# Optimization experiments

Hardware: AMD Instinct MI355X
Metric: run time of the kernel (lower is better)

## Reference

```python
import jax, jax.numpy as jnp
import numpy as np

MIN_FP16 = -65504.0  # torch.finfo(torch.float16).min
D_MODEL = 2048
NUM_HEAD = 16
HEAD_SIZE = D_MODEL // NUM_HEAD


def setup_inputs() -> dict:
    key = jax.random.key(0)
    k1, k2, k3, k4, k5 = jax.random.split(key, 5)
    B, S, D = 4, 2048, D_MODEL
    scale_in = 1.0 / np.sqrt(D)
    return {
        "x": jax.random.normal(k1, (B, S, D), dtype=jnp.float32),
        # nn.Linear(d_model, 3*d_model): weight [3D, D], bias [3D]
        "w_proj": jax.random.normal(k2, (3 * D, D), dtype=jnp.float32) * scale_in,
        "b_proj": jax.random.normal(k3, (3 * D,), dtype=jnp.float32) * 0.01,
        # nn.Linear(d_model, d_model)
        "w_ff": jax.random.normal(k4, (D, D), dtype=jnp.float32) * scale_in,
        "b_ff": jax.random.normal(k5, (D,), dtype=jnp.float32) * 0.01,
    }


def reference(x, w_proj, b_proj, w_ff, b_ff):
    B, S, D = x.shape
    H, hs = NUM_HEAD, HEAD_SIZE
    # fused QKV projection: [B,S,3D]
    x_proj = jnp.einsum("bsd,ed->bse", x, w_proj) + b_proj
    # view [B,S,H,3*hs] -> [B,H,S,3*hs], split into q,k,v [B,H,S,hs]
    x_proj = x_proj.reshape(B, S, H, 3 * hs).transpose(0, 2, 1, 3)
    q, k, v = jnp.split(x_proj, 3, axis=-1)
    next_prefix_kv = jnp.stack((k, v))  # [2,B,H,S,hs]
    # scaled scores [B,H,S,S]
    scores = jnp.einsum("bhqd,bhkd->bhqk", q, k) / np.sqrt(hs)
    # causal mask (prefix_kv=None => tmp_len == seq_len, offset 0)
    causal = jnp.tril(jnp.ones((S, S), dtype=bool))
    scores = jnp.where(causal, scores, MIN_FP16)
    probs = jax.nn.softmax(scores, axis=-1)  # dropout p=0 (eval)
    attn_o = jnp.einsum("bhqk,bhkd->bhqd", probs, v)
    attn_o = attn_o.transpose(0, 2, 1, 3).reshape(B, S, D)
    ff_o = jnp.einsum("bsd,ed->bse", attn_o, w_ff) + b_ff
    return ff_o, next_prefix_kv
```

## Files before the change

kernel.cpp:

```cpp
#include <hip/hip_runtime.h>


using floatx4 = __attribute__((ext_vector_type(4))) float;
using short8  = __attribute__((ext_vector_type(8))) short;

#define MFMA_BF16(a, b, c) __builtin_amdgcn_mfma_f32_16x16x32_bf16((a), (b), (c), 0, 0, 0)

static __device__ __forceinline__ unsigned short f2bf(float f) {
    unsigned u = __float_as_uint(f);
    u += 0x7FFF + ((u >> 16) & 1);
    return (unsigned short)(u >> 16);
}
static __device__ __forceinline__ short8 cvt8(const float* p) {
    float4 a = ((const float4*)p)[0];
    float4 b = ((const float4*)p)[1];
    short8 r;
    r[0] = (short)f2bf(a.x); r[1] = (short)f2bf(a.y);
    r[2] = (short)f2bf(a.z); r[3] = (short)f2bf(a.w);
    r[4] = (short)f2bf(b.x); r[5] = (short)f2bf(b.y);
    r[6] = (short)f2bf(b.z); r[7] = (short)f2bf(b.w);
    return r;
}

static __device__ __forceinline__ void gld16(const void* g, const void* l) {
    unsigned loff = (unsigned)__builtin_amdgcn_readfirstlane((int)(unsigned)(uintptr_t)l);
    __builtin_amdgcn_global_load_lds(
        (__attribute__((address_space(1))) unsigned*)(uintptr_t)g,
        (__attribute__((address_space(3))) unsigned*)loff,
        16, 0, 0);
}

__global__ __launch_bounds__(256) void cvt_kernel(
    const float* __restrict__ X, const float* __restrict__ Wp,
    unsigned short* __restrict__ Xb, unsigned short* __restrict__ Wpb)
{
    const int NX = 2097152;
    const int NP = 1572864;
    const int total = NX + NP;
    const int stride = gridDim.x * 256;
    for (int g = blockIdx.x * 256 + threadIdx.x; g < total; g += stride) {
        const float* src; unsigned short* dst; int off;
        if (g < NX) { src = X;  dst = Xb;  off = g; }
        else        { src = Wp; dst = Wpb; off = g - NX; }
        const int row = off >> 8;
        const int c   = off & 255;
        const int dof = (row << 8) | (c & ~7) | ((c ^ row) & 7);
        short8 v = cvt8(src + (size_t)off * 8);
        *(short8*)(dst + (size_t)dof * 8) = v;
    }
}

__global__ __launch_bounds__(256) void gemm_qkv_kernel(
    const unsigned short* __restrict__ Xb,
    const unsigned short* __restrict__ Wpb,
    const float* __restrict__ Bias,
    unsigned short* __restrict__ Qws,
    float* __restrict__ KV)
{
    const int K = 2048;
    __shared__ unsigned short As[128 * 64];
    __shared__ unsigned short Bs[128 * 64];
    const int n0 = blockIdx.x * 128;
    const int m0 = blockIdx.y * 128;
    const int t = threadIdx.x;
    const int w = t >> 6, l = t & 63;
    const int lr = l & 15, lq = l >> 4;
    const int lr7 = lr & 7;
    const int wr = w >> 1, wc = w & 1;
    const int srow = l >> 3;
    const int scol = (l & 7) * 8;

    floatx4 acc[4][4];
#pragma unroll
    for (int mi = 0; mi < 4; ++mi)
#pragma unroll
        for (int ni = 0; ni < 4; ++ni) acc[mi][ni] = (floatx4){0, 0, 0, 0};

    for (int k0 = 0; k0 < K; k0 += 64) {
        __syncthreads();
#pragma unroll
        for (int i = 0; i < 4; ++i) {
            const int rb = (i * 4 + w) * 8;
            gld16(Xb  + (size_t)(m0 + rb + srow) * K + k0 + scol, &As[(rb)*64]);
            gld16(Wpb + (size_t)(n0 + rb + srow) * K + k0 + scol, &Bs[(rb)*64]);
        }
        __syncthreads();
#pragma unroll
        for (int kc = 0; kc < 2; ++kc) {
            short8 af[4], bg[4];
#pragma unroll
            for (int mi = 0; mi < 4; ++mi)
                af[mi] = *(const short8*)
                    &As[(wr * 64 + mi * 16 + lr) * 64 + ((((kc << 2) | lq) ^ lr7) << 3)];
#pragma unroll
            for (int ni = 0; ni < 4; ++ni)
                bg[ni] = *(const short8*)
                    &Bs[(wc * 64 + ni * 16 + lr) * 64 + ((((kc << 2) | lq) ^ lr7) << 3)];
#pragma unroll
            for (int mi = 0; mi < 4; ++mi)
#pragma unroll
                for (int ni = 0; ni < 4; ++ni)
                    acc[mi][ni] = MFMA_BF16(af[mi], bg[ni], acc[mi][ni]);
        }
    }
#pragma unroll
    for (int ni = 0; ni < 4; ++ni) {
        int e = n0 + wc * 64 + ni * 16 + lr;
        int h = e / 384;
        int c = e - h * 384;
        float bias = Bias[e];
#pragma unroll
        for (int mi = 0; mi < 4; ++mi) {
#pragma unroll
            for (int r = 0; r < 4; ++r) {
                int m = m0 + wr * 64 + mi * 16 + lq * 4 + r;
                int b = m >> 11, s = m & 2047;
                float o = acc[mi][ni][r] + bias;
                size_t base = (((size_t)(b * 16 + h)) * 2048 + s) * 128;
                if (c < 128)
                    Qws[base + ((((c >> 3) ^ (s & 7)) << 3) | (c & 7))] = f2bf(o);
                else if (c < 256) KV[base + (c - 128)] = o;
                else              KV[(size_t)16777216 + base + (c - 256)] = o;
            }
        }
    }
}

__global__ __launch_bounds__(256) void repack_kv_kernel(
    const float* __restrict__ KV,
    unsigned short* __restrict__ Kb,
    unsigned short* __restrict__ Vtb)
{
    __shared__ short Vt[128][72];
    const int bh = blockIdx.x >> 5;
    const int w  = blockIdx.x & 31;
    const int t  = threadIdx.x;

    {
        const int kr = t >> 2;
        const int c4 = (t & 3) * 4;
        const int s  = w * 64 + kr;
        const float* kp = KV + ((size_t)bh * 2048 + s) * 128 + c4 * 8;
        unsigned short* ko = Kb + ((size_t)bh * 2048 + s) * 128;
        const int sw = s & 7;
#pragma unroll
        for (int j = 0; j < 4; ++j) {
            short8 v = cvt8(kp + j * 8);
            *(short8*)(ko + ((c4 + j) ^ sw) * 8) = v;
        }
    }

    {
        const int vkp = t & 31;
        const int vd0 = (t >> 5) * 16;
        const float* vap = KV + (((size_t)64 + bh) * 2048 + w * 64 + 2 * vkp) * 128 + vd0;
        short8 va0 = cvt8(vap),       va1 = cvt8(vap + 8);
        short8 vb0 = cvt8(vap + 128), vb1 = cvt8(vap + 136);
#pragma unroll
        for (int dd = 0; dd < 8; ++dd) {
            unsigned w0 = (unsigned)(unsigned short)va0[dd] |
                          ((unsigned)(unsigned short)vb0[dd] << 16);
            unsigned w1 = (unsigned)(unsigned short)va1[dd] |
                          ((unsigned)(unsigned short)vb1[dd] << 16);
            *(unsigned*)&Vt[vd0 + dd][2 * vkp]     = w0;
            *(unsigned*)&Vt[vd0 + 8 + dd][2 * vkp] = w1;
        }
    }
    __syncthreads();
    {
        const int d = t >> 1, hf = t & 1;
        unsigned short* vo = Vtb + ((size_t)bh * 128 + d) * 2048 + w * 64;
        const int dw = d & 7;
#pragma unroll
        for (int j = 0; j < 4; ++j) {
            int c = hf * 4 + j;
            uint4 v = *(const uint4*)&Vt[d][c * 8];
            *(uint4*)(vo + (c ^ dw) * 8) = v;
        }
    }
}

__global__ __launch_bounds__(256) void attn_kernel(
    unsigned short* __restrict__ QA,
    const unsigned short* __restrict__ Kb,
    const unsigned short* __restrict__ Vtb)
{
    const int S = 2048;
    __shared__ unsigned short Ks[2][64 * 128];
    __shared__ unsigned short Vt[2][128 * 64];
    __shared__ short Pb[4][16][72];

    const int bh = blockIdx.y;
    const int qt = gridDim.x - 1 - blockIdx.x;
    const int q0 = qt * 64;
    const int t = threadIdx.x;
    const int wv = t >> 6;
    const int l = t & 63;
    const int lr = l & 15;
    const int lq = l >> 4;
    const int lr7 = lr & 7;

    unsigned short* Qp = QA + ((size_t)bh * S + q0) * 128;
    const unsigned short* gK = Kb + (size_t)bh * S * 128;
    const unsigned short* gV = Vtb + (size_t)bh * 128 * S;

    short8 qf[4];
#pragma unroll
    for (int kc = 0; kc < 4; ++kc)
        qf[kc] = *(const short8*)(Qp + (size_t)(wv * 16 + lr) * 128 +
                                  ((((kc << 2) | lq) ^ lr7) << 3));

    float m_i = -1e30f, l_i = 0.0f;
    floatx4 oacc[8];
#pragma unroll
    for (int nt = 0; nt < 8; ++nt) oacc[nt] = (floatx4){0, 0, 0, 0};

    const int ntiles = qt + 1;

#define STAGE(BUF, KV0)                                                        \
    {                                                                          \
        const int kv0_ = (KV0);                                                \
        _Pragma("unroll")                                                      \
        for (int i = 0; i < 4; ++i) {                                          \
            const int off = (i * 16 + wv * 4) * 128;                           \
            gld16(gK + (size_t)kv0_ * 128 + off + l * 8, &Ks[BUF][off]);       \
        }                                                                      \
        _Pragma("unroll")                                                      \
        for (int i = 0; i < 4; ++i) {                                          \
            const int ob = (i * 16 + wv * 4) * 256 + l * 16;                   \
            const int d = ob >> 7, rem = ob & 127;                             \
            gld16((const char*)gV + (size_t)d * (S * 2) + kv0_ * 2 + rem,      \
                  (const char*)&Vt[BUF][0] + (i * 16 + wv * 4) * 256);         \
        }                                                                      \
    }

    STAGE(0, 0);

    for (int it = 0; it < ntiles; ++it) {
        const int cur = it & 1;
        __syncthreads();
        if (it + 1 < ntiles) STAGE(cur ^ 1, (it + 1) * 64);

        const unsigned short* Kc = &Ks[cur][0];
        const unsigned short* Vc = &Vt[cur][0];

        floatx4 sacc[4];
#pragma unroll
        for (int mt = 0; mt < 4; ++mt) sacc[mt] = (floatx4){0, 0, 0, 0};
#pragma unroll
        for (int kc = 0; kc < 4; ++kc) {
#pragma unroll
            for (int mt = 0; mt < 4; ++mt) {
                short8 a = *(const short8*)
                    &Kc[(mt * 16 + lr) * 128 + ((((kc << 2) | lq) ^ lr7) << 3)];
                sacc[mt] = MFMA_BF16(a, qf[kc], sacc[mt]);
            }
        }

        float sv[16];
        const bool diag = (it == qt);
#pragma unroll
        for (int mt = 0; mt < 4; ++mt)
#pragma unroll
            for (int r = 0; r < 4; ++r) {
                float x = sacc[mt][r] * 0.08838834764831845f;
                if (diag && (mt * 16 + lq * 4 + r > wv * 16 + lr)) x = -1e30f;
                sv[mt * 4 + r] = x;
            }
        float mx = sv[0];
#pragma unroll
        for (int j = 1; j < 16; ++j) mx = fmaxf(mx, sv[j]);
        mx = fmaxf(mx, __shfl_xor(mx, 16));
        mx = fmaxf(mx, __shfl_xor(mx, 32));
        float m_new = fmaxf(m_i, mx);
        float alpha = __expf(m_i - m_new);
        m_i = m_new;
        float sum = 0.0f;
        unsigned pw[8];
#pragma unroll
        for (int j = 0; j < 8; ++j) {
            float p0 = __expf(sv[2 * j]     - m_new);
            float p1 = __expf(sv[2 * j + 1] - m_new);
            sum += p0 + p1;
            pw[j] = (unsigned)f2bf(p0) | ((unsigned)f2bf(p1) << 16);
        }
        sum += __shfl_xor(sum, 16);
        sum += __shfl_xor(sum, 32);
        l_i = l_i * alpha + sum;

#pragma unroll
        for (int mt = 0; mt < 4; ++mt)
            *(uint2*)&Pb[wv][lr][mt * 16 + lq * 4] =
                make_uint2(pw[2 * mt], pw[2 * mt + 1]);

        float am[4];
#pragma unroll
        for (int r = 0; r < 4; ++r) am[r] = __shfl(alpha, lq * 4 + r);
#pragma unroll
        for (int nt = 0; nt < 8; ++nt)
#pragma unroll
            for (int r = 0; r < 4; ++r) oacc[nt][r] *= am[r];

        short8 pa0 = *(const short8*)&Pb[wv][lr][lq * 8];
        short8 pa1 = *(const short8*)&Pb[wv][lr][32 + lq * 8];
#pragma unroll
        for (int nt = 0; nt < 8; ++nt) {
            const int row = nt * 16 + lr;
            short8 v0 = *(const short8*)&Vc[row * 64 + ((lq ^ lr7) << 3)];
            short8 v1 = *(const short8*)&Vc[row * 64 + (((4 + lq) ^ lr7) << 3)];
            oacc[nt] = MFMA_BF16(pa0, v0, oacc[nt]);
            oacc[nt] = MFMA_BF16(pa1, v1, oacc[nt]);
        }
    }
#undef STAGE

    float lm[4];
#pragma unroll
    for (int r = 0; r < 4; ++r) lm[r] = 1.0f / __shfl(l_i, lq * 4 + r);
#pragma unroll
    for (int nt = 0; nt < 8; ++nt) {
#pragma unroll
        for (int r = 0; r < 4; ++r) {
            int q = wv * 16 + lq * 4 + r;
            int ch = (nt * 2 + (lr >> 3)) ^ (q & 7);
            Qp[(size_t)q * 128 + (ch << 3) + (lr & 7)] = f2bf(oacc[nt][r] * lm[r]);
        }
    }
}

__global__ __launch_bounds__(256) void gemm_ff_kernel(
    const unsigned short* __restrict__ AOhm,
    const float* __restrict__ W,
    const float* __restrict__ Bias,
    float* __restrict__ Out)
{
    const int K = 2048;
    __shared__ unsigned short As[128 * 64];
    __shared__ unsigned short Bs[128 * 64];
    const int n0 = blockIdx.x * 128;
    const int m0 = blockIdx.y * 128;
    const int t = threadIdx.x;
    const int w = t >> 6, l = t & 63;
    const int lr = l & 15, lq = l >> 4;
    const int lr7 = lr & 7;
    const int wr = w >> 1, wc = w & 1;
    const int srow = l >> 3;
    const int scol = (l & 7) * 8;

    const int brow = t >> 1;
    const int bch0 = (t & 1) * 4;
    const int bsw  = brow & 7;
    const float* gB = W + (size_t)(n0 + brow) * K + bch0 * 8;

    floatx4 acc[4][4];
#pragma unroll
    for (int mi = 0; mi < 4; ++mi)
#pragma unroll
        for (int ni = 0; ni < 4; ++ni) acc[mi][ni] = (floatx4){0, 0, 0, 0};

    for (int k0 = 0; k0 < K; k0 += 64) {
        short8 bc[4];
#pragma unroll
        for (int j = 0; j < 4; ++j) bc[j] = cvt8(gB + k0 + j * 8);

        const int h = k0 >> 7, d0 = (k0 & 127) + scol;
        __syncthreads();
#pragma unroll
        for (int i = 0; i < 4; ++i) {
            const int rb = (i * 4 + w) * 8;
            const int m = m0 + rb + srow;
            const int b = m >> 11, s = m & 2047;
            gld16(AOhm + ((size_t)(b * 16 + h) * 2048 + s) * 128 + d0, &As[(rb)*64]);
        }
#pragma unroll
        for (int j = 0; j < 4; ++j)
            *(short8*)&Bs[brow * 64 + (((bch0 + j) ^ bsw) << 3)] = bc[j];
        __syncthreads();
#pragma unroll
        for (int kc = 0; kc < 2; ++kc) {
            short8 af[4], bg[4];
#pragma unroll
            for (int mi = 0; mi < 4; ++mi)
                af[mi] = *(const short8*)
                    &As[(wr * 64 + mi * 16 + lr) * 64 + ((((kc << 2) | lq) ^ lr7) << 3)];
#pragma unroll
            for (int ni = 0; ni < 4; ++ni)
                bg[ni] = *(const short8*)
                    &Bs[(wc * 64 + ni * 16 + lr) * 64 + ((((kc << 2) | lq) ^ lr7) << 3)];
#pragma unroll
            for (int mi = 0; mi < 4; ++mi)
#pragma unroll
                for (int ni = 0; ni < 4; ++ni)
                    acc[mi][ni] = MFMA_BF16(af[mi], bg[ni], acc[mi][ni]);
        }
    }
#pragma unroll
    for (int ni = 0; ni < 4; ++ni) {
        int e = n0 + wc * 64 + ni * 16 + lr;
        float bias = Bias[e];
#pragma unroll
        for (int mi = 0; mi < 4; ++mi) {
#pragma unroll
            for (int r = 0; r < 4; ++r) {
                int m = m0 + wr * 64 + mi * 16 + lq * 4 + r;
                Out[(size_t)m * 2048 + e] = acc[mi][ni][r] + bias;
            }
        }
    }
}

extern "C" void kernel_launch(void* const* d_in, const int* in_sizes, int n_in,
                              void* d_out, int out_size, void* d_ws, size_t ws_size,
                              hipStream_t stream) {
    const float* X  = (const float*)d_in[0];
    const float* Wp = (const float*)d_in[1];
    const float* bp = (const float*)d_in[2];
    const float* Wf = (const float*)d_in[3];
    const float* bf = (const float*)d_in[4];

    float* out = (float*)d_out;
    float* kv  = out + 16777216;
    unsigned short* Qws = (unsigned short*)d_ws;

    unsigned short* Xb  = (unsigned short*)out;
    unsigned short* Wpb = Xb + 16777216;
    unsigned short* Kbs = (unsigned short*)out;
    unsigned short* Vtb = Kbs + 16777216;

    cvt_kernel<<<dim3(2048), 256, 0, stream>>>(X, Wp, Xb, Wpb);
    gemm_qkv_kernel<<<dim3(48, 64), 256, 0, stream>>>(Xb, Wpb, bp, Qws, kv);
    repack_kv_kernel<<<dim3(2048), 256, 0, stream>>>(kv, Kbs, Vtb);
    attn_kernel<<<dim3(32, 64), 256, 0, stream>>>(Qws, Kbs, Vtb);
    gemm_ff_kernel<<<dim3(16, 64), 256, 0, stream>>>(Qws, Wf, bf, out);
}
```

Baseline: 962.4 us.

## Pre-convert FF weights to bf16, add lazy softmax rescale, packed bf16 conversion

Several changes land together. The cvt kernel now also converts w_ff to swizzled bf16 in workspace when there is room, so the FF GEMM can load both operands with global-to-LDS copies instead of converting fp32 on the fly; the old kernel is kept as a fallback. Attention skips the output rescale when the wave's new row max is within 8 of the running max (lazy rescaling) and uses hardware packed bf16 conversion. K/V staging addresses are precomputed as incrementing offsets. The lazy rescale allows unnormalised exponentials up to e^8, which slightly changes numerics but should stay within bf16 range.

Result: faster. 887.8 us (-7.8%).

```diff
diff --git a/kernel.cpp b/kernel.cpp
--- a/kernel.cpp
+++ b/kernel.cpp
@@ -1,4 +1,5 @@
 #include <hip/hip_runtime.h>
+#include <hip/hip_bf16.h>
 
 
 using floatx4 = __attribute__((ext_vector_type(4))) float;
@@ -11,15 +12,18 @@
     u += 0x7FFF + ((u >> 16) & 1);
     return (unsigned short)(u >> 16);
 }
+static __device__ __forceinline__ unsigned cvtpk(float lo, float hi) {
+    union { __hip_bfloat162 h; unsigned u; } r;
+    r.h = __float22bfloat162_rn(make_float2(lo, hi));
+    return r.u;
+}
 static __device__ __forceinline__ short8 cvt8(const float* p) {
     float4 a = ((const float4*)p)[0];
     float4 b = ((const float4*)p)[1];
-    short8 r;
-    r[0] = (short)f2bf(a.x); r[1] = (short)f2bf(a.y);
-    r[2] = (short)f2bf(a.z); r[3] = (short)f2bf(a.w);
-    r[4] = (short)f2bf(b.x); r[5] = (short)f2bf(b.y);
-    r[6] = (short)f2bf(b.z); r[7] = (short)f2bf(b.w);
-    return r;
+    union { unsigned u[4]; short8 s; } r;
+    r.u[0] = cvtpk(a.x, a.y); r.u[1] = cvtpk(a.z, a.w);
+    r.u[2] = cvtpk(b.x, b.y); r.u[3] = cvtpk(b.z, b.w);
+    return r.s;
 }
 
 static __device__ __forceinline__ void gld16(const void* g, const void* l) {
@@ -32,16 +36,20 @@
 
 __global__ __launch_bounds__(256) void cvt_kernel(
     const float* __restrict__ X, const float* __restrict__ Wp,
-    unsigned short* __restrict__ Xb, unsigned short* __restrict__ Wpb)
+    const float* __restrict__ Wf,
+    unsigned short* __restrict__ Xb, unsigned short* __restrict__ Wpb,
+    unsigned short* __restrict__ Wfb, int doWf)
 {
     const int NX = 2097152;
     const int NP = 1572864;
-    const int total = NX + NP;
+    const int NF = 524288;
+    const int total = NX + NP + (doWf ? NF : 0);
     const int stride = gridDim.x * 256;
     for (int g = blockIdx.x * 256 + threadIdx.x; g < total; g += stride) {
         const float* src; unsigned short* dst; int off;
-        if (g < NX) { src = X;  dst = Xb;  off = g; }
-        else        { src = Wp; dst = Wpb; off = g - NX; }
+        if (g < NX)           { src = X;  dst = Xb;  off = g; }
+        else if (g < NX + NP) { src = Wp; dst = Wpb; off = g - NX; }
+        else                  { src = Wf; dst = Wfb; off = g - NX - NP; }
         const int row = off >> 8;
         const int c   = off & 255;
         const int dof = (row << 8) | (c & ~7) | ((c ^ row) & 7);
@@ -215,31 +223,33 @@
 #pragma unroll
     for (int nt = 0; nt < 8; ++nt) oacc[nt] = (floatx4){0, 0, 0, 0};
 
-    const int ntiles = qt + 1;
-
-#define STAGE(BUF, KV0)                                                        \
+    const unsigned short* gKl = gK + l * 8;
+    const char* gVl = (const char*)gV + (size_t)((l >> 3) * 4096 + (l & 7) * 16);
+    size_t tK = 0, tV = 0;
+
+#define STAGE(BUF)                                                             \
     {                                                                          \
-        const int kv0_ = (KV0);                                                \
         _Pragma("unroll")                                                      \
         for (int i = 0; i < 4; ++i) {                                          \
             const int off = (i * 16 + wv * 4) * 128;                           \
-            gld16(gK + (size_t)kv0_ * 128 + off + l * 8, &Ks[BUF][off]);       \
+            gld16(gKl + tK + off, &Ks[BUF][off]);                              \
         }                                                                      \
         _Pragma("unroll")                                                      \
         for (int i = 0; i < 4; ++i) {                                          \
-            const int ob = (i * 16 + wv * 4) * 256 + l * 16;                   \
-            const int d = ob >> 7, rem = ob & 127;                             \
-            gld16((const char*)gV + (size_t)d * (S * 2) + kv0_ * 2 + rem,      \
+            const int vb = (i * 32 + wv * 8) * 4096;                           \
+            gld16(gVl + tV + vb,                                               \
                   (const char*)&Vt[BUF][0] + (i * 16 + wv * 4) * 256);         \
         }                                                                      \
     }
 
-    STAGE(0, 0);
+    const int ntiles = qt + 1;
+    STAGE(0);
+    tK += 8192; tV += 128;
 
     for (int it = 0; it < ntiles; ++it) {
         const int cur = it & 1;
         __syncthreads();
-        if (it + 1 < ntiles) STAGE(cur ^ 1, (it + 1) * 64);
+        if (it + 1 < ntiles) { STAGE(cur ^ 1); tK += 8192; tV += 128; }
 
         const unsigned short* Kc = &Ks[cur][0];
         const unsigned short* Vc = &Vt[cur][0];
@@ -272,17 +282,28 @@
         for (int j = 1; j < 16; ++j) mx = fmaxf(mx, sv[j]);
         mx = fmaxf(mx, __shfl_xor(mx, 16));
         mx = fmaxf(mx, __shfl_xor(mx, 32));
-        float m_new = fmaxf(m_i, mx);
-        float alpha = __expf(m_i - m_new);
-        m_i = m_new;
+        const bool nores = __all(mx <= m_i + 8.0f) != 0;
+        float alpha = 1.0f;
+        if (!nores) {
+            float m_new = fmaxf(m_i, mx);
+            alpha = __expf(m_i - m_new);
+            m_i = m_new;
+            float am[4];
+#pragma unroll
+            for (int r = 0; r < 4; ++r) am[r] = __shfl(alpha, lq * 4 + r);
+#pragma unroll
+            for (int nt = 0; nt < 8; ++nt)
+#pragma unroll
+                for (int r = 0; r < 4; ++r) oacc[nt][r] *= am[r];
+        }
         float sum = 0.0f;
         unsigned pw[8];
 #pragma unroll
         for (int j = 0; j < 8; ++j) {
-            float p0 = __expf(sv[2 * j]     - m_new);
-            float p1 = __expf(sv[2 * j + 1] - m_new);
+            float p0 = __expf(sv[2 * j]     - m_i);
+            float p1 = __expf(sv[2 * j + 1] - m_i);
             sum += p0 + p1;
-            pw[j] = (unsigned)f2bf(p0) | ((unsigned)f2bf(p1) << 16);
+            pw[j] = cvtpk(p0, p1);
         }
         sum += __shfl_xor(sum, 16);
         sum += __shfl_xor(sum, 32);
@@ -292,14 +313,6 @@
         for (int mt = 0; mt < 4; ++mt)
             *(uint2*)&Pb[wv][lr][mt * 16 + lq * 4] =
                 make_uint2(pw[2 * mt], pw[2 * mt + 1]);
-
-        float am[4];
-#pragma unroll
-        for (int r = 0; r < 4; ++r) am[r] = __shfl(alpha, lq * 4 + r);
-#pragma unroll
-        for (int nt = 0; nt < 8; ++nt)
-#pragma unroll
-            for (int r = 0; r < 4; ++r) oacc[nt][r] *= am[r];
 
         short8 pa0 = *(const short8*)&Pb[wv][lr][lq * 8];
         short8 pa1 = *(const short8*)&Pb[wv][lr][32 + lq * 8];
@@ -329,6 +342,76 @@
 }
 
 __global__ __launch_bounds__(256) void gemm_ff_kernel(
+    const unsigned short* __restrict__ AOhm,
+    const unsigned short* __restrict__ Wfb,
+    const float* __restrict__ Bias,
+    float* __restrict__ Out)
+{
+    const int K = 2048;
+    __shared__ unsigned short As[128 * 64];
+    __shared__ unsigned short Bs[128 * 64];
+    const int n0 = blockIdx.x * 128;
+    const int m0 = blockIdx.y * 128;
+    const int t = threadIdx.x;
+    const int w = t >> 6, l = t & 63;
+    const int lr = l & 15, lq = l >> 4;
+    const int lr7 = lr & 7;
+    const int wr = w >> 1, wc = w & 1;
+    const int srow = l >> 3;
+    const int scol = (l & 7) * 8;
+
+    floatx4 acc[4][4];
+#pragma unroll
+    for (int mi = 0; mi < 4; ++mi)
+#pragma unroll
+        for (int ni = 0; ni < 4; ++ni) acc[mi][ni] = (floatx4){0, 0, 0, 0};
+
+    for (int k0 = 0; k0 < K; k0 += 64) {
+        const int h = k0 >> 7, d0 = (k0 & 127) + scol;
+        __syncthreads();
+#pragma unroll
+        for (int i = 0; i < 4; ++i) {
+            const int rb = (i * 4 + w) * 8;
+            const int m = m0 + rb + srow;
+            const int b = m >> 11, s = m & 2047;
+            gld16(AOhm + ((size_t)(b * 16 + h) * 2048 + s) * 128 + d0, &As[(rb)*64]);
+            gld16(Wfb  + (size_t)(n0 + rb + srow) * K + k0 + scol,     &Bs[(rb)*64]);
+        }
+        __syncthreads();
+#pragma unroll
+        for (int kc = 0; kc < 2; ++kc) {
+            short8 af[4], bg[4];
+#pragma unroll
+            for (int mi = 0; mi < 4; ++mi)
+                af[mi] = *(const short8*)
+                    &As[(wr * 64 + mi * 16 + lr) * 64 + ((((kc << 2) | lq) ^ lr7) << 3)];
+#pragma unroll
+            for (int ni = 0; ni < 4; ++ni)
+                bg[ni] = *(const short8*)
+                    &Bs[(wc * 64 + ni * 16 + lr) * 64 + ((((kc << 2) | lq) ^ lr7) << 3)];
+#pragma unroll
+            for (int mi = 0; mi < 4; ++mi)
+#pragma unroll
+                for (int ni = 0; ni < 4; ++ni)
+                    acc[mi][ni] = MFMA_BF16(af[mi], bg[ni], acc[mi][ni]);
+        }
+    }
+#pragma unroll
+    for (int ni = 0; ni < 4; ++ni) {
+        int e = n0 + wc * 64 + ni * 16 + lr;
+        float bias = Bias[e];
+#pragma unroll
+        for (int mi = 0; mi < 4; ++mi) {
+#pragma unroll
+            for (int r = 0; r < 4; ++r) {
+                int m = m0 + wr * 64 + mi * 16 + lq * 4 + r;
+                Out[(size_t)m * 2048 + e] = acc[mi][ni][r] + bias;
+            }
+        }
+    }
+}
+
+__global__ __launch_bounds__(256) void gemm_ff_fb_kernel(
     const unsigned short* __restrict__ AOhm,
     const float* __restrict__ W,
     const float* __restrict__ Bias,
@@ -426,10 +509,16 @@
     unsigned short* Wpb = Xb + 16777216;
     unsigned short* Kbs = (unsigned short*)out;
     unsigned short* Vtb = Kbs + 16777216;
-
-    cvt_kernel<<<dim3(2048), 256, 0, stream>>>(X, Wp, Xb, Wpb);
+    const bool wfInWs = ws_size >= (size_t)33554432 + 8388608;
+    unsigned short* Wfb = wfInWs ? Qws + 16777216 : (unsigned short*)nullptr;
+
+    cvt_kernel<<<dim3(2048), 256, 0, stream>>>(X, Wp, Wf, Xb, Wpb, Wfb,
+                                               wfInWs ? 1 : 0);
     gemm_qkv_kernel<<<dim3(48, 64), 256, 0, stream>>>(Xb, Wpb, bp, Qws, kv);
     repack_kv_kernel<<<dim3(2048), 256, 0, stream>>>(kv, Kbs, Vtb);
     attn_kernel<<<dim3(32, 64), 256, 0, stream>>>(Qws, Kbs, Vtb);
-    gemm_ff_kernel<<<dim3(16, 64), 256, 0, stream>>>(Qws, Wf, bf, out);
-}
+    if (wfInWs)
+        gemm_ff_kernel<<<dim3(16, 64), 256, 0, stream>>>(Qws, Wfb, bf, out);
+    else
+        gemm_ff_fb_kernel<<<dim3(16, 64), 256, 0, stream>>>(Qws, Wf, bf, out);
+}
```
